# Performance work log

Measured on AMD Instinct MI355X. Metric: run time of the kernel, lower is better.

The kernel has to match this reference:

```python
import jax, jax.numpy as jnp
import numpy as np

DIM = 1024
N_HEADS = 16
HEAD_DIM = DIM // N_HEADS
EPS = 1e-05
ROPE_BASE = 1000000.0


def apply_rope(x, base=ROPE_BASE):
    # x: [b, seq, heads, head_dim]
    b, seq, n_heads, dim = x.shape
    half = dim // 2
    i = jnp.arange(half)
    theta = 1.0 / base ** (2 * i / dim)
    pos = jnp.arange(seq)
    angles = pos[:, None] * theta[None, :]            # [seq, half]
    cos = jnp.cos(angles)[None, :, None, :]           # [1, seq, 1, half]
    sin = jnp.sin(angles)[None, :, None, :]
    x1, x2 = jnp.split(x, 2, axis=-1)
    return jnp.concatenate([x1 * cos - x2 * sin, x1 * sin + x2 * cos], axis=-1)


def setup_inputs() -> dict:
    key = jax.random.key(0)
    ks = jax.random.split(key, 6)
    b, seq = 2, 2048
    scale = 1.0 / np.sqrt(DIM)
    x = jax.random.normal(ks[0], (b, seq, DIM), dtype=jnp.float32)
    w_norm = jnp.ones((DIM,), dtype=jnp.float32)
    Wq = jax.random.normal(ks[1], (DIM, DIM), dtype=jnp.float32) * scale
    Wk = jax.random.normal(ks[2], (DIM, DIM), dtype=jnp.float32) * scale
    Wv = jax.random.normal(ks[3], (DIM, DIM), dtype=jnp.float32) * scale
    Wo = jax.random.normal(ks[4], (DIM, DIM), dtype=jnp.float32) * scale
    return {"x": x, "w_norm": w_norm, "Wq": Wq, "Wk": Wk, "Wv": Wv, "Wo": Wo}


def reference(x, w_norm, Wq, Wk, Wv, Wo):
    b, seq, d = x.shape
    # RMSNorm
    rms = jnp.sqrt(jnp.mean(x * x, axis=-1, keepdims=True) + EPS)
    x_norm = x / rms * w_norm
    # QKV projections (Dense without bias: y = x @ W)
    q = (x_norm @ Wq).reshape(b, seq, N_HEADS, HEAD_DIM)
    k = (x_norm @ Wk).reshape(b, seq, N_HEADS, HEAD_DIM)
    v = (x_norm @ Wv).reshape(b, seq, N_HEADS, HEAD_DIM)
    q = apply_rope(q)
    k = apply_rope(k)
    # Causal attention with full [b,h,t,s] scores (faithful to source)
    scores = jnp.einsum('bthd,bshd->bhts', q, k) / jnp.sqrt(jnp.float32(HEAD_DIM))
    causal = jnp.triu(jnp.full((seq, seq), -jnp.inf, dtype=scores.dtype), k=1)
    scores = scores + causal[None, None, :, :]
    attn = jax.nn.softmax(scores, axis=-1)
    out = jnp.einsum('bhts,bshd->bthd', attn, v).reshape(b, seq, d)
    return out @ Wo
```

## Files before the change

### kernel.cpp

```cpp
#include <hip/hip_runtime.h>

#define DIM 1024
#define SEQ 2048
#define BATCH 2
#define NHEADS 16
#define HD 64
#define ROWS (BATCH * SEQ)

typedef __bf16 bf16x8 __attribute__((ext_vector_type(8)));
typedef __bf16 bf16x4 __attribute__((ext_vector_type(4)));
typedef float f32x4 __attribute__((ext_vector_type(4)));
typedef float f32x16 __attribute__((ext_vector_type(16)));
typedef unsigned u32x4 __attribute__((ext_vector_type(4)));

__device__ __forceinline__ f32x4 f4zero() {
    f32x4 z = {0.f, 0.f, 0.f, 0.f};
    return z;
}

__device__ __forceinline__ unsigned cvtpk(float lo, float hi) {
    unsigned r;
    asm("v_cvt_pk_bf16_f32 %0, %1, %2" : "=v"(r) : "v"(lo), "v"(hi));
    return r;
}

__device__ __forceinline__ void pl32swap(unsigned& a, unsigned& b) {
    asm volatile("v_permlane32_swap_b32 %0, %1" : "+v"(a), "+v"(b));
}

__device__ __forceinline__ float fexp2(float x) {
    float r;
    asm("v_exp_f32 %0, %1" : "=v"(r) : "v"(x));
    return r;
}

#define GLOAD_LDS16(g, l)                                                                  \
    __builtin_amdgcn_global_load_lds((const __attribute__((address_space(1))) void*)(g),   \
                                     (__attribute__((address_space(3))) void*)(l), 16, 0, 0)

__global__ __launch_bounds__(256) void rmsnorm_bf16(const float* __restrict__ x,
                                                    const float* __restrict__ w,
                                                    __bf16* __restrict__ xn) {
    int row = blockIdx.x;
    int t = threadIdx.x;
    float4 v = ((const float4*)(x + (size_t)row * DIM))[t];
    float ss = v.x * v.x + v.y * v.y + v.z * v.z + v.w * v.w;
#pragma unroll
    for (int off = 1; off < 64; off <<= 1) ss += __shfl_xor(ss, off);
    __shared__ float red[4];
    if ((t & 63) == 0) red[t >> 6] = ss;
    __syncthreads();
    ss = red[0] + red[1] + red[2] + red[3];
    float scale = rsqrtf(ss * (1.0f / DIM) + 1e-5f);
    float4 wv = ((const float4*)w)[t];
    bf16x4 o;
    o[0] = (__bf16)(v.x * scale * wv.x);
    o[1] = (__bf16)(v.y * scale * wv.y);
    o[2] = (__bf16)(v.z * scale * wv.z);
    o[3] = (__bf16)(v.w * scale * wv.w);
    *(bf16x4*)(xn + (size_t)row * DIM + t * 4) = o;
}

__global__ __launch_bounds__(256) void wcvt_kernel(const float* __restrict__ Wq,
                                                   const float* __restrict__ Wk,
                                                   const float* __restrict__ Wv,
                                                   const float* __restrict__ Wo,
                                                   __bf16* tq, __bf16* tk, __bf16* tv, __bf16* to_) {
    int z = blockIdx.z;
    const float* W = z == 0 ? Wq : z == 1 ? Wk : z == 2 ? Wv : Wo;
    __bf16* T = z == 0 ? tq : z == 1 ? tk : z == 2 ? tv : to_;
    __shared__ float tile[32][33];
    int n0 = blockIdx.x * 32, k0 = blockIdx.y * 32;
    int tx = threadIdx.x & 31, ty = threadIdx.x >> 5;
#pragma unroll
    for (int j = 0; j < 32; j += 8) tile[ty + j][tx] = W[(size_t)(k0 + ty + j) * DIM + n0 + tx];
    __syncthreads();
#pragma unroll
    for (int j = 0; j < 32; j += 8)
        T[(size_t)(n0 + ty + j) * DIM + k0 + tx] = (__bf16)tile[tx][ty + j];
}

__global__ __launch_bounds__(256) void rope_table_kernel(float* __restrict__ cosT,
                                                         float* __restrict__ sinT) {
    int idx = blockIdx.x * 256 + threadIdx.x;
    int s = idx >> 5, i = idx & 31;
    float e = (2.0f * (float)i) / 64.0f;
    float theta = 1.0f / powf(1000000.0f, e);
    float ang = (float)s * theta;
    cosT[idx] = cosf(ang);
    sinT[idx] = sinf(ang);
}

__device__ __forceinline__ void gemm_core64(const __bf16* __restrict__ A,
                                            const __bf16* __restrict__ Bt,
                                            int K, __bf16* As, __bf16* Bs,
                                            f32x4 (&acc)[4][4], int row0, int col0) {
    int tid = threadIdx.x;
    int w = tid >> 6, l = tid & 63, l15 = l & 15, g = l >> 4;
    int wr = (w >> 1) << 6, wc = (w & 1) << 6;

    int srow = tid >> 3;
    int schunk = ((tid & 7) ^ (srow & 7)) << 3;
    const __bf16* gA = A + (size_t)(row0 + srow) * K + schunk;
    const __bf16* gB = Bt + (size_t)(col0 + srow) * K + schunk;
    __bf16* lA = As + w * 512;
    __bf16* lB = Bs + w * 512;

#pragma unroll
    for (int i = 0; i < 4; ++i)
#pragma unroll
        for (int j = 0; j < 4; ++j) acc[i][j] = f4zero();

    int xr = (l15 & 7);
    for (int k0 = 0; k0 < K; k0 += 64) {
        __syncthreads();
#pragma unroll
        for (int c = 0; c < 4; ++c) {
            GLOAD_LDS16(gA + (size_t)(c * 32) * K + k0, lA + c * 2048);
            GLOAD_LDS16(gB + (size_t)(c * 32) * K + k0, lB + c * 2048);
        }
        __syncthreads();
#pragma unroll
        for (int kk = 0; kk < 2; ++kk) {
            int q8 = kk * 4 + g;
            int rc = (q8 ^ xr) << 3;
            bf16x8 af[4], bfr[4];
#pragma unroll
            for (int i = 0; i < 4; ++i)
                af[i] = *(const bf16x8*)&As[(wr + i * 16 + l15) * 64 + rc];
#pragma unroll
            for (int j = 0; j < 4; ++j)
                bfr[j] = *(const bf16x8*)&Bs[(wc + j * 16 + l15) * 64 + rc];
            __builtin_amdgcn_s_setprio(1);
#pragma unroll
            for (int i = 0; i < 4; ++i)
#pragma unroll
                for (int j = 0; j < 4; ++j)
                    acc[i][j] = __builtin_amdgcn_mfma_f32_16x16x32_bf16(af[i], bfr[j], acc[i][j], 0, 0, 0);
            __builtin_amdgcn_s_setprio(0);
        }
    }
}

__global__ __launch_bounds__(256) void gemm_qkv_kernel(const __bf16* __restrict__ xn,
                                                       const __bf16* __restrict__ wq,
                                                       const __bf16* __restrict__ wk,
                                                       const __bf16* __restrict__ wv,
                                                       __bf16* __restrict__ qf,
                                                       __bf16* __restrict__ kf,
                                                       __bf16* __restrict__ vf,
                                                       const float* __restrict__ cosT,
                                                       const float* __restrict__ sinT) {
    __shared__ __bf16 smem[16384];
    __bf16* As = smem;
    __bf16* Bs = smem + 8192;
    int bid0 = blockIdx.x;
    int bid = ((bid0 & 7) * 96) + (bid0 >> 3);
    int tid = threadIdx.x;
    int w = tid >> 6, l = tid & 63, l15 = l & 15, gq = l >> 4;
    int l31 = l & 31, hi = l >> 5;
    int wr = (w >> 1) << 6, wc = (w & 1) << 6;
    __bf16* Ls = smem + w * 2304;
    f32x4 acc[4][4];

    if (bid < 512) {
        int z = bid >> 8, t = bid & 255;
        int col0 = (t & 7) << 7, row0 = (t >> 3) << 7;
        gemm_core64(xn, z ? wk : wq, DIM, As, Bs, acc, row0, col0);
        __syncthreads();
        __bf16* F = z ? kf : qf;
        int colbase = col0 + wc;
        int hh = colbase >> 6;
        int row0w = row0 + wr;
        int bb = row0w >> 11;
        int bh = bb * 16 + hh;
        int tbase = (row0w & (SEQ - 1)) >> 5;
#pragma unroll
        for (int p = 0; p < 2; ++p) {
#pragma unroll
            for (int i = 0; i < 4; ++i) {
#pragma unroll
                for (int r = 0; r < 4; ++r) {
                    int row64 = i * 16 + gq * 4 + r;
                    int s = (row0w + row64) & (SEQ - 1);
#pragma unroll
                    for (int jj = 0; jj < 2; ++jj) {
                        float c = cosT[s * 32 + jj * 16 + l15];
                        float sn = sinT[s * 32 + jj * 16 + l15];
                        float val;
                        if (p == 0)
                            val = acc[i][jj][r] * c - acc[i][jj + 2][r] * sn;
                        else
                            val = acc[i][jj][r] * sn + acc[i][jj + 2][r] * c;
                        Ls[row64 * 36 + jj * 16 + l15] = (__bf16)val;
                    }
                }
            }
#pragma unroll
            for (int si = 0; si < 2; ++si) {
#pragma unroll
                for (int gg = 0; gg < 2; ++gg) {
                    int g = 2 * p + gg;
                    bf16x8 v = *(const bf16x8*)&Ls[(si * 32 + l31) * 36 + gg * 16 + hi * 8];
                    size_t dst = (((size_t)(bh * 64 + tbase + si) * 4 + g) * 64 + l) * 8;
                    __builtin_nontemporal_store(v, (bf16x8*)&F[dst]);
                }
            }
        }
    } else {
        int t = bid - 512;
        int b = t >> 7, r7 = t & 127;
        int row0 = (r7 >> 4) << 7;
        int col0 = (r7 & 15) << 7;
        gemm_core64(wv, xn + (size_t)b * SEQ * DIM, DIM, As, Bs, acc, row0, col0);
        __syncthreads();
        int hh = (row0 + wr) >> 6;
        int bh = b * 16 + hh;
#pragma unroll
        for (int p = 0; p < 2; ++p) {
#pragma unroll
            for (int i = 0; i < 4; ++i) {
#pragma unroll
                for (int r = 0; r < 4; ++r) {
                    int row64 = i * 16 + gq * 4 + r;
#pragma unroll
                    for (int jj = 0; jj < 2; ++jj)
                        Ls[row64 * 36 + jj * 16 + l15] = (__bf16)acc[i][2 * p + jj][r];
                }
            }
            int t32 = ((col0 + wc) >> 5) + p;
#pragma unroll
            for (int half = 0; half < 2; ++half) {
#pragma unroll
                for (int kk = 0; kk < 2; ++kk) {
                    bf16x8 v = *(const bf16x8*)&Ls[(half * 32 + l31) * 36 + kk * 16 + hi * 8];
                    size_t dst = ((((size_t)(bh * 64 + t32) * 2 + half) * 2 + kk) * 64 + l) * 8;
                    __builtin_nontemporal_store(v, (bf16x8*)&vf[dst]);
                }
            }
        }
    }
}

__global__ __launch_bounds__(256) void gemm_out_kernel(const __bf16* __restrict__ ctx,
                                                       const __bf16* __restrict__ wo,
                                                       float* __restrict__ out) {
    __shared__ __bf16 As[8192];
    __shared__ __bf16 Bs[8192];
    int b0 = blockIdx.x;
    int t = ((b0 & 7) * 32) + (b0 >> 3);
    int row0 = (t >> 3) << 7, col0 = (t & 7) << 7;
    f32x4 acc[4][4];
    gemm_core64(ctx, wo, DIM, As, Bs, acc, row0, col0);
    int tid = threadIdx.x;
    int w = tid >> 6, l = tid & 63, l15 = l & 15, g = l >> 4;
    int wr = (w >> 1) << 6, wc = (w & 1) << 6;
#pragma unroll
    for (int i = 0; i < 4; ++i)
#pragma unroll
        for (int j = 0; j < 4; ++j)
#pragma unroll
            for (int r = 0; r < 4; ++r) {
                int row = row0 + wr + i * 16 + g * 4 + r;
                int col = col0 + wc + j * 16 + l15;
                __builtin_nontemporal_store(acc[i][j][r], &out[(size_t)row * DIM + col]);
            }
}

__global__ __launch_bounds__(256, 3) void attn_mfma_kernel(const __bf16* __restrict__ qf,
                                                           const __bf16* __restrict__ kf,
                                                           const __bf16* __restrict__ vf,
                                                           __bf16* __restrict__ part_O,
                                                           float* __restrict__ part_ml) {
    int bh = blockIdx.x;
    int tid = threadIdx.x, wvx = tid >> 6, l = tid & 63;
    int wslot = (int)blockIdx.y * 4 + wvx;
    int slot = 95 - wslot;
    int qp, ci;
    if (slot < 32) {
        qp = slot;
        ci = 0;
    } else {
        int t = slot - 32;
        qp = 32 + (t >> 1);
        ci = t & 1;
    }
    int rem = qp - (ci << 5);
    int ntiles = rem < 32 ? rem + 1 : 32;
    int dtile = rem < 32 ? rem : -1;
    int t0 = ci << 5;

    int l31 = l & 31, hi = l >> 5;
    int qrow = qp * 32 + l31;

    bf16x8 qfr[4];
    {
        const __bf16* qp_ = qf + ((size_t)bh * 64 + qp) * 2048 + (size_t)l * 8;
        const float c2 = 0.125f * 1.44269504f;
#pragma unroll
        for (int g = 0; g < 4; ++g) {
            bf16x8 tq = *(const bf16x8*)(qp_ + g * 512);
#pragma unroll
            for (int e = 0; e < 8; ++e) qfr[g][e] = (__bf16)((float)tq[e] * c2);
        }
    }

    const __bf16* kfp = kf + ((size_t)bh * 64 + t0) * 2048 + (size_t)l * 8;
    const __bf16* vfp = vf + ((size_t)bh * 64 + t0) * 2048 + (size_t)l * 8;

    f32x16 oA, oB;
#pragma unroll
    for (int r = 0; r < 16; ++r) {
        oA[r] = 0.f;
        oB[r] = 0.f;
    }
    float m_run = -1e30f, l_run = 0.f;

    bf16x8 ka[4], kb[4];
#pragma unroll
    for (int g = 0; g < 4; ++g) ka[g] = *(const bf16x8*)(kfp + g * 512);

    auto tile_body = [&](bf16x8 (&kcur)[4], bf16x8 (&knxt)[4], int st) {
        if (st + 1 < ntiles) {
            const __bf16* kn = kfp + (size_t)(st + 1) * 2048;
#pragma unroll
            for (int g = 0; g < 4; ++g) knxt[g] = *(const bf16x8*)(kn + g * 512);
        }
        const __bf16* vp = vfp + (size_t)st * 2048;
        bf16x8 v00 = *(const bf16x8*)(vp);
        bf16x8 v01 = *(const bf16x8*)(vp + 512);
        bf16x8 v10 = *(const bf16x8*)(vp + 1024);
        bf16x8 v11 = *(const bf16x8*)(vp + 1536);

        f32x16 sa;
#pragma unroll
        for (int r = 0; r < 16; ++r) sa[r] = 0.f;
        __builtin_amdgcn_s_setprio(1);
#pragma unroll
        for (int g = 0; g < 4; ++g)
            sa = __builtin_amdgcn_mfma_f32_32x32x16_bf16(kcur[g], qfr[g], sa, 0, 0, 0);
        __builtin_amdgcn_s_setprio(0);

        if (st == dtile) {
            int s0 = (t0 + st) << 5;
#pragma unroll
            for (int r = 0; r < 16; ++r) {
                int kg = s0 + (r & 3) + 8 * (r >> 2) + 4 * hi;
                if (kg > qrow) sa[r] = -1e30f;
            }
        }

        float mx[8];
#pragma unroll
        for (int r = 0; r < 8; ++r) mx[r] = fmaxf(sa[r], sa[r + 8]);
#pragma unroll
        for (int r = 0; r < 4; ++r) mx[r] = fmaxf(mx[r], mx[r + 4]);
        float lmax = fmaxf(fmaxf(mx[0], mx[1]), fmaxf(mx[2], mx[3]));
        if (!__all(lmax <= m_run + 10.0f)) {
            float omax = fmaxf(lmax, __shfl_xor(lmax, 32));
            float m_new = fmaxf(m_run, omax);
            float alpha = fexp2(m_run - m_new);
            l_run *= alpha;
#pragma unroll
            for (int r = 0; r < 16; ++r) {
                oA[r] *= alpha;
                oB[r] *= alpha;
            }
            m_run = m_new;
        }
#pragma unroll
        for (int r = 0; r < 16; ++r) sa[r] = fexp2(sa[r] - m_run);
        float s8[8];
#pragma unroll
        for (int r = 0; r < 8; ++r) s8[r] = sa[r] + sa[r + 8];
#pragma unroll
        for (int r = 0; r < 4; ++r) s8[r] += s8[r + 4];
        float ls = (s8[0] + s8[1]) + (s8[2] + s8[3]);
        l_run += ls + __shfl_xor(ls, 32);

        unsigned a0 = cvtpk(sa[0], sa[1]), b0 = cvtpk(sa[4], sa[5]);
        pl32swap(a0, b0);
        unsigned c0 = cvtpk(sa[2], sa[3]), d0 = cvtpk(sa[6], sa[7]);
        pl32swap(c0, d0);
        u32x4 t4a = {a0, c0, b0, d0};
        bf16x8 pa0 = __builtin_bit_cast(bf16x8, t4a);
        unsigned a1 = cvtpk(sa[8], sa[9]), b1 = cvtpk(sa[12], sa[13]);
        pl32swap(a1, b1);
        unsigned c1 = cvtpk(sa[10], sa[11]), d1 = cvtpk(sa[14], sa[15]);
        pl32swap(c1, d1);
        u32x4 t4b = {a1, c1, b1, d1};
        bf16x8 pa1 = __builtin_bit_cast(bf16x8, t4b);

        __builtin_amdgcn_s_setprio(1);
        oA = __builtin_amdgcn_mfma_f32_32x32x16_bf16(v00, pa0, oA, 0, 0, 0);
        oA = __builtin_amdgcn_mfma_f32_32x32x16_bf16(v01, pa1, oA, 0, 0, 0);
        oB = __builtin_amdgcn_mfma_f32_32x32x16_bf16(v10, pa0, oB, 0, 0, 0);
        oB = __builtin_amdgcn_mfma_f32_32x32x16_bf16(v11, pa1, oB, 0, 0, 0);
        __builtin_amdgcn_s_setprio(0);
    };

    int st = 0;
    while (st < ntiles) {
        tile_body(ka, kb, st);
        ++st;
        if (st >= ntiles) break;
        tile_body(kb, ka, st);
        ++st;
    }

    int gslot = bh * 96 + slot;
    __bf16* po = part_O + (size_t)gslot * 2048 + l31 * 64;
#pragma unroll
    for (int rr = 0; rr < 16; rr += 4) {
        int d0 = 8 * (rr >> 2) + 4 * hi;
        uint2 pA = {cvtpk(oA[rr], oA[rr + 1]), cvtpk(oA[rr + 2], oA[rr + 3])};
        uint2 pB = {cvtpk(oB[rr], oB[rr + 1]), cvtpk(oB[rr + 2], oB[rr + 3])};
        *(uint2*)&po[d0] = pA;
        *(uint2*)&po[32 + d0] = pB;
    }
    if (hi == 0) {
        part_ml[(size_t)gslot * 64 + l31] = m_run;
        part_ml[(size_t)gslot * 64 + 32 + l31] = l_run;
    }
}

__global__ __launch_bounds__(128) void attn_combine_kernel(const __bf16* __restrict__ part_O,
                                                           const float* __restrict__ part_ml,
                                                           __bf16* __restrict__ ctx) {
    int bh = blockIdx.x, qp = blockIdx.y;
    int b = bh >> 4, h = bh & 15;
    int nch = 1 + (qp >> 5);
    int base = qp < 32 ? qp : 32 + 2 * (qp - 32);
    size_t so = (size_t)bh * 96 + base;
    int t = threadIdx.x;
    int row = t >> 2, dseg = (t & 3) << 4;

    float mv0 = part_ml[so * 64 + row];
    float mv1 = -1e30f;
    if (nch > 1) mv1 = part_ml[(so + 1) * 64 + row];
    float mmax = fmaxf(mv0, mv1);

    float acc[16];
#pragma unroll
    for (int e = 0; e < 16; ++e) acc[e] = 0.f;
    float lsum = 0.f;

#pragma unroll 2
    for (int i = 0; i < 2; ++i) {
        if (i >= nch) break;
        float mi = i == 0 ? mv0 : mv1;
        float wsc = fexp2(mi - mmax);
        lsum += wsc * part_ml[(so + i) * 64 + 32 + row];
        const __bf16* po = part_O + (so + i) * 2048 + row * 64 + dseg;
        bf16x8 a = *(const bf16x8*)po;
        bf16x8 b2 = *(const bf16x8*)(po + 8);
#pragma unroll
        for (int e = 0; e < 8; ++e) {
            acc[e] += wsc * (float)a[e];
            acc[8 + e] += wsc * (float)b2[e];
        }
    }

    float inv = 1.0f / lsum;
    bf16x8 oa, ob;
#pragma unroll
    for (int e = 0; e < 8; ++e) {
        oa[e] = (__bf16)(acc[e] * inv);
        ob[e] = (__bf16)(acc[8 + e] * inv);
    }
    size_t off = ((size_t)(b * SEQ) + qp * 32 + row) * DIM + h * HD + dseg;
    *(bf16x8*)&ctx[off] = oa;
    *(bf16x8*)&ctx[off + 8] = ob;
}

extern "C" void kernel_launch(void* const* d_in, const int* in_sizes, int n_in,
                              void* d_out, int out_size, void* d_ws, size_t ws_size,
                              hipStream_t stream) {
    const float* x = (const float*)d_in[0];
    const float* w_norm = (const float*)d_in[1];
    const float* Wq = (const float*)d_in[2];
    const float* Wk = (const float*)d_in[3];
    const float* Wv = (const float*)d_in[4];
    const float* Wo = (const float*)d_in[5];
    float* out = (float*)d_out;
    char* w8 = (char*)d_ws;

    const size_t MB = 1ull << 20;
    __bf16* xn = (__bf16*)(w8);
    __bf16* wtq = (__bf16*)(w8 + 8 * MB);
    __bf16* wtk = (__bf16*)(w8 + 10 * MB);
    __bf16* wtv = (__bf16*)(w8 + 12 * MB);
    __bf16* part_O = (__bf16*)(w8);
    float* part_ml = (float*)(w8 + 12 * MB);
    __bf16* wto = (__bf16*)(w8 + 14 * MB);
    __bf16* qf = (__bf16*)(w8 + 16 * MB);
    __bf16* kf = (__bf16*)(w8 + 24 * MB);
    __bf16* vf = (__bf16*)(w8 + 32 * MB);
    __bf16* ctx = (__bf16*)(w8 + 40 * MB);
    float* cosT = (float*)(w8 + 48 * MB);
    float* sinT = cosT + SEQ * 32;

    wcvt_kernel<<<dim3(32, 32, 4), 256, 0, stream>>>(Wq, Wk, Wv, Wo, wtq, wtk, wtv, wto);
    rmsnorm_bf16<<<ROWS, 256, 0, stream>>>(x, w_norm, xn);
    rope_table_kernel<<<(SEQ * 32) / 256, 256, 0, stream>>>(cosT, sinT);

    gemm_qkv_kernel<<<768, 256, 0, stream>>>(xn, wtq, wtk, wtv, qf, kf, vf, cosT, sinT);

    attn_mfma_kernel<<<dim3(BATCH * NHEADS, 24), 256, 0, stream>>>(qf, kf, vf, part_O, part_ml);
    attn_combine_kernel<<<dim3(BATCH * NHEADS, SEQ / 32), 128, 0, stream>>>(part_O, part_ml, ctx);

    gemm_out_kernel<<<256, 256, 0, stream>>>(ctx, wto, out);
}
```

Measured before the change: 134.3 us.

## Split causal attention KV range into 16-tile chunks with finer work slots

Attention work is re-partitioned so each wave handles at most 16 KV tiles instead of 32, giving 160 slots per batch-head (up to 4 chunks per query block) in place of 96. Blocks shrink to 128 threads, the grid becomes 1-D with a remapping of the batch-head index, and the combine kernel merges up to four partial results. The aim is better load balance and occupancy across CUs. The cost is more partial-output traffic and extra combine work, and the workspace layout is shifted to make room for the larger partial buffers.

```diff
diff --git a/kernel.cpp b/kernel.cpp
--- a/kernel.cpp
+++ b/kernel.cpp
@@ -267,28 +267,37 @@
             }
 }
 
-__global__ __launch_bounds__(256, 3) void attn_mfma_kernel(const __bf16* __restrict__ qf,
+__global__ __launch_bounds__(128, 5) void attn_mfma_kernel(const __bf16* __restrict__ qf,
                                                            const __bf16* __restrict__ kf,
                                                            const __bf16* __restrict__ vf,
                                                            __bf16* __restrict__ part_O,
                                                            float* __restrict__ part_ml) {
-    int bh = blockIdx.x;
+    int bid = blockIdx.x;
+    int bh = (bid & 7) | (((bid >> 3) & 3) << 3);
+    int rest = bid >> 5;
     int tid = threadIdx.x, wvx = tid >> 6, l = tid & 63;
-    int wslot = (int)blockIdx.y * 4 + wvx;
-    int slot = 95 - wslot;
+    int slot = 159 - (rest * 2 + wvx);
     int qp, ci;
-    if (slot < 32) {
+    if (slot < 16) {
         qp = slot;
         ci = 0;
+    } else if (slot < 48) {
+        int t = slot - 16;
+        qp = 16 + (t >> 1);
+        ci = t & 1;
+    } else if (slot < 96) {
+        int t = slot - 48;
+        qp = 32 + t / 3;
+        ci = t - 3 * (t / 3);
     } else {
-        int t = slot - 32;
-        qp = 32 + (t >> 1);
-        ci = t & 1;
-    }
-    int rem = qp - (ci << 5);
-    int ntiles = rem < 32 ? rem + 1 : 32;
-    int dtile = rem < 32 ? rem : -1;
-    int t0 = ci << 5;
+        int t = slot - 96;
+        qp = 48 + (t >> 2);
+        ci = t & 3;
+    }
+    int rem = qp - (ci << 4);
+    int ntiles = rem < 16 ? rem + 1 : 16;
+    int dtile = rem < 16 ? rem : -1;
+    int t0 = ci << 4;
 
     int l31 = l & 31, hi = l >> 5;
     int qrow = qp * 32 + l31;
@@ -408,7 +417,7 @@
         ++st;
     }
 
-    int gslot = bh * 96 + slot;
+    int gslot = bh * 160 + slot;
     __bf16* po = part_O + (size_t)gslot * 2048 + l31 * 64;
 #pragma unroll
     for (int rr = 0; rr < 16; rr += 4) {
@@ -429,26 +438,32 @@
                                                            __bf16* __restrict__ ctx) {
     int bh = blockIdx.x, qp = blockIdx.y;
     int b = bh >> 4, h = bh & 15;
-    int nch = 1 + (qp >> 5);
-    int base = qp < 32 ? qp : 32 + 2 * (qp - 32);
-    size_t so = (size_t)bh * 96 + base;
+    int nch = 1 + (qp >> 4);
+    int base;
+    if (qp < 16) base = qp;
+    else if (qp < 32) base = 16 + 2 * (qp - 16);
+    else if (qp < 48) base = 48 + 3 * (qp - 32);
+    else base = 96 + 4 * (qp - 48);
+    size_t so = (size_t)bh * 160 + base;
     int t = threadIdx.x;
     int row = t >> 2, dseg = (t & 3) << 4;
 
-    float mv0 = part_ml[so * 64 + row];
-    float mv1 = -1e30f;
+    float mv0 = part_ml[(so + 0) * 64 + row];
+    float mv1 = -1e30f, mv2 = -1e30f, mv3 = -1e30f;
     if (nch > 1) mv1 = part_ml[(so + 1) * 64 + row];
-    float mmax = fmaxf(mv0, mv1);
+    if (nch > 2) mv2 = part_ml[(so + 2) * 64 + row];
+    if (nch > 3) mv3 = part_ml[(so + 3) * 64 + row];
+    float mmax = fmaxf(fmaxf(mv0, mv1), fmaxf(mv2, mv3));
 
     float acc[16];
 #pragma unroll
     for (int e = 0; e < 16; ++e) acc[e] = 0.f;
     float lsum = 0.f;
 
-#pragma unroll 2
-    for (int i = 0; i < 2; ++i) {
+#pragma unroll 4
+    for (int i = 0; i < 4; ++i) {
         if (i >= nch) break;
-        float mi = i == 0 ? mv0 : mv1;
+        float mi = i == 0 ? mv0 : i == 1 ? mv1 : i == 2 ? mv2 : mv3;
         float wsc = fexp2(mi - mmax);
         lsum += wsc * part_ml[(so + i) * 64 + 32 + row];
         const __bf16* po = part_O + (so + i) * 2048 + row * 64 + dseg;
@@ -491,13 +506,13 @@
     __bf16* wtk = (__bf16*)(w8 + 10 * MB);
     __bf16* wtv = (__bf16*)(w8 + 12 * MB);
     __bf16* part_O = (__bf16*)(w8);
-    float* part_ml = (float*)(w8 + 12 * MB);
-    __bf16* wto = (__bf16*)(w8 + 14 * MB);
-    __bf16* qf = (__bf16*)(w8 + 16 * MB);
-    __bf16* kf = (__bf16*)(w8 + 24 * MB);
-    __bf16* vf = (__bf16*)(w8 + 32 * MB);
-    __bf16* ctx = (__bf16*)(w8 + 40 * MB);
-    float* cosT = (float*)(w8 + 48 * MB);
+    float* part_ml = (float*)(w8 + 20 * MB);
+    __bf16* wto = (__bf16*)(w8 + 22 * MB);
+    __bf16* qf = (__bf16*)(w8 + 24 * MB);
+    __bf16* kf = (__bf16*)(w8 + 32 * MB);
+    __bf16* vf = (__bf16*)(w8 + 40 * MB);
+    __bf16* ctx = (__bf16*)(w8 + 48 * MB);
+    float* cosT = (float*)(w8 + 56 * MB);
     float* sinT = cosT + SEQ * 32;
 
     wcvt_kernel<<<dim3(32, 32, 4), 256, 0, stream>>>(Wq, Wk, Wv, Wo, wtq, wtk, wtv, wto);
@@ -506,7 +521,7 @@
 
     gemm_qkv_kernel<<<768, 256, 0, stream>>>(xn, wtq, wtk, wtv, qf, kf, vf, cosT, sinT);
 
-    attn_mfma_kernel<<<dim3(BATCH * NHEADS, 24), 256, 0, stream>>>(qf, kf, vf, part_O, part_ml);
+    attn_mfma_kernel<<<2560, 128, 0, stream>>>(qf, kf, vf, part_O, part_ml);
     attn_combine_kernel<<<dim3(BATCH * NHEADS, SEQ / 32), 128, 0, stream>>>(part_O, part_ml, ctx);
 
     gemm_out_kernel<<<256, 256, 0, stream>>>(ctx, wto, out);
```

Result: slower. 321.7 us (+139.4%).
